# Optimization experiments

Measured on AMD Instinct MI355X. Metric: run time of the kernel, lower is better.

The kernel has to match this reference:

```python
import jax, jax.numpy as jnp
import numpy as np

D = 128  # time-encoder dimension == attention embed_dim


def harmonic_encode(ts, basis_freq):
    # ts: (N,) -> (N, D); phases are zero in the original module
    m = ts[:, None] * basis_freq[None, :]
    return jnp.sqrt(1.0 / D) * jnp.concatenate([jnp.cos(m), jnp.sin(m)], axis=1)


def mha_1head(q, k, mask, Wq, bq, Wk, bk, Wv, bv, Wo, bo):
    # Single-head nn.MultiheadAttention. q: (T, D) queries (torch batch dim),
    # k: (S, D) shared keys/values (original repeats these T times; same math),
    # mask: (T, S) True = masked out (key_padding_mask semantics).
    qp = q @ Wq.T + bq
    kp = k @ Wk.T + bk
    vp = k @ Wv.T + bv
    scores = jnp.einsum('td,sd->ts', qp, kp) / jnp.sqrt(jnp.asarray(D, q.dtype))
    scores = jnp.where(mask, -jnp.inf, scores)
    attn = jax.nn.softmax(scores, axis=-1)  # (T, S)
    return (attn @ vp) @ Wo.T + bo


def setup_inputs() -> dict:
    key = jax.random.key(0)
    ks = jax.random.split(key, 24)
    T, L, V = 4096, 8192, 1000
    s = 1.0 / np.sqrt(D)
    inp = {
        't': jax.random.uniform(ks[0], (T,), jnp.float32),
        'e_nodes_ts': jax.random.uniform(ks[1], (L,), jnp.float32),
        'e_nodes_exp': jax.random.randint(ks[2], (L,), 0, V),
        'e_node_target': jax.random.randint(ks[3], (1,), 0, V),
        'basis_freq': jnp.asarray(1.0 / 5.0 ** np.linspace(1, 9, D // 2), jnp.float32),
        'phi': jnp.ones((1,), jnp.float32),
        'W_lin': jax.random.normal(ks[4], (1, 2 * D), jnp.float32) * 0.05,
        'b_lin': jnp.zeros((1,), jnp.float32),
    }
    kidx = 5
    for suf in ('_s', '_n'):
        for nm in ('Wq', 'Wk', 'Wv', 'Wo'):
            inp[nm + suf] = jax.random.normal(ks[kidx], (D, D), jnp.float32) * s
            kidx += 1
        for nm in ('bq', 'bk', 'bv', 'bo'):
            inp[nm + suf] = jnp.zeros((D,), jnp.float32)
    return inp


def reference(t, e_nodes_ts, e_nodes_exp, e_node_target, basis_freq, phi, W_lin, b_lin,
              Wq_s, Wk_s, Wv_s, Wo_s, bq_s, bk_s, bv_s, bo_s,
              Wq_n, Wk_n, Wv_n, Wo_n, bq_n, bk_n, bv_n, bo_n):
    # prepend sentinels exactly as the torch forward does
    ts_all = jnp.concatenate([jnp.zeros((2,), e_nodes_ts.dtype), e_nodes_ts])      # (S,)
    exp_all = jnp.concatenate([jnp.full((1,), -1, e_nodes_exp.dtype), e_node_target, e_nodes_exp])  # (S,)

    phi_t = harmonic_encode(t, basis_freq)        # (T, D)
    phi_ts = harmonic_encode(ts_all, basis_freq)  # (S, D)

    pad = ts_all[None, :] > t[:, None]            # (T, S) future events masked
    self_mask = pad | (exp_all != e_node_target[0])[None, :]
    neig_mask = pad | (exp_all == e_node_target[0])[None, :]

    out_s = mha_1head(phi_t, phi_ts, self_mask, Wq_s, bq_s, Wk_s, bk_s, Wv_s, bv_s, Wo_s, bo_s)
    out_n = mha_1head(phi_t, phi_ts, neig_mask, Wq_n, bq_n, Wk_n, bk_n, Wv_n, bv_n, Wo_n, bo_n)
    atten_output = jnp.concatenate([out_s, out_n], axis=1)  # (T, 2D)

    lam = atten_output @ W_lin.T + b_lin          # (T, 1)
    x = lam * phi
    x = jnp.where(x > 20.0, 20.0, x)              # clamp as in soft_plus()
    lambdav = (1.0 / phi) * jnp.log1p(jnp.exp(x))
    return lambdav, atten_output
```

## Files before the change

kernel.cpp:

```cpp
#include <hip/hip_runtime.h>

#define T_Q 4096
#define S_TOT 8194
#define S_ALLOC 8256
#define SELF_CAP 128
#define NSEG 11
#define NSLOT 12
#define NTILE_N 129
#define SCALE 0.08838834764831843f
#define NEG_BIG -1.0e30f
#define TS_INF 3.0e38f

typedef __attribute__((ext_vector_type(8))) short short8;
typedef __attribute__((ext_vector_type(4))) float f32x4;
typedef __attribute__((ext_vector_type(4))) unsigned short ush4;
typedef unsigned short ush;
typedef unsigned int uint32;
typedef unsigned long long u64;

static __device__ __forceinline__ ush f2bf(float f) {
    unsigned int u = __float_as_uint(f);
    u += 0x7FFFu + ((u >> 16) & 1u);
    return (ush)(u >> 16);
}

__global__ __launch_bounds__(256) void prep_kernel(
    const float* __restrict__ t, const float* __restrict__ ets,
    const int* __restrict__ exps, const int* __restrict__ tgtp,
    const float* __restrict__ bf,
    const float* __restrict__ Wo_s, const float* __restrict__ Wv_s, const float* __restrict__ bv_s,
    const float* __restrict__ Wo_n, const float* __restrict__ Wv_n, const float* __restrict__ bv_n,
    const float* __restrict__ Wq_s, const float* __restrict__ Wq_n,
    const float* __restrict__ Wk_s, const float* __restrict__ Wk_n,
    ush* __restrict__ phi_t, ush* __restrict__ phi_ts,
    float* __restrict__ ts_pad, float* __restrict__ ts1, int* __restrict__ perm1,
    u64* __restrict__ maskbits, ush* __restrict__ Wb, float* __restrict__ bvo)
{
    __shared__ float red[256];
    __shared__ int swcnt[4];
    __shared__ int stot;
    int bid = blockIdx.x, tid = threadIdx.x;

    if (bid < 3088) {
        int R = bid * 4 + (tid >> 6);
        int j = tid & 63;
        float x; ush* dst;
        if (R < T_Q) { x = t[R]; dst = phi_t + (size_t)R * 128; }
        else {
            int s = R - T_Q;
            x = (s < 2) ? 0.0f : ((s < S_TOT) ? ets[s - 2] : 0.0f);
            dst = phi_ts + (size_t)s * 128;
        }
        float m = x * bf[j];
        dst[j]      = f2bf(cosf(m) * SCALE);
        dst[64 + j] = f2bf(sinf(m) * SCALE);
    } else if (bid == 3088) {
        int tgt = tgtp[0];
        for (int i = tid; i < S_ALLOC; i += 256)
            ts_pad[i] = (i < 2) ? 0.f : ((i < S_TOT) ? ets[i - 2] : TS_INF);
        int w4 = tid >> 6, lane = tid & 63;
        int cbeg = w4 * 33, cend = (w4 == 3) ? NTILE_N : (cbeg + 33);
        u64 ltm = ((u64)1 << lane) - 1ull;
        int cnt = 0;
        for (int ch = cbeg; ch < cend; ++ch) {
            int s = ch * 64 + lane;
            bool m = (s < S_TOT) && ((s == 1) || (s >= 2 && exps[s - 2] == tgt));
            u64 b = __ballot(m);
            if (lane == 0) maskbits[ch] = b;
            cnt += __popcll(b);
        }
        if (lane == 0) swcnt[w4] = cnt;
        __syncthreads();
        if (tid == 0) {
            int a = 0;
            #pragma unroll
            for (int i = 0; i < 4; ++i) { int tc = swcnt[i]; swcnt[i] = a; a += tc; }
            stot = a;
        }
        __syncthreads();
        int off2 = swcnt[w4];
        for (int ch = cbeg; ch < cend; ++ch) {
            int s = ch * 64 + lane;
            bool m = (s < S_TOT) && ((s == 1) || (s >= 2 && exps[s - 2] == tgt));
            u64 b = __ballot(m);
            if (m) {
                int p = off2 + __popcll(b & ltm);
                if (p < SELF_CAP) { perm1[p] = s; ts1[p] = (s >= 2) ? ets[s - 2] : 0.f; }
            }
            off2 += __popcll(b);
        }
        __syncthreads();
        int st = stot > SELF_CAP ? SELF_CAP : stot;
        for (int i = st + tid; i < SELF_CAP; i += 256) { perm1[i] = 0; ts1[i] = TS_INF; }
    } else if (bid < 3217) {
        int row = bid - 3089;
        int h = tid >> 7, col = tid & 127;
        const float* Wo = h ? Wo_n : Wo_s;
        const float* Wv = h ? Wv_n : Wv_s;
        const float* bv = h ? bv_n : bv_s;
        float acc = 0.f;
        for (int jj = 0; jj < 128; ++jj) acc += Wo[row * 128 + jj] * Wv[jj * 128 + col];
        Wb[(size_t)(4 + h) * 16384 + row * 128 + col] = f2bf(acc);
        red[tid] = Wo[row * 128 + col] * bv[col];
        __syncthreads();
        for (int off = 64; off > 0; off >>= 1) {
            if ((tid & 127) < off) red[tid] += red[tid + off];
            __syncthreads();
        }
        if ((tid & 127) == 0) bvo[h * 128 + row] = red[tid];
    } else {
        int idx = (bid - 3217) * 256 + tid;
        int which = idx >> 14, e = idx & 16383;
        const float* src;
        switch (which) {
            case 0: src = Wq_s; break; case 1: src = Wq_n; break;
            case 2: src = Wk_s; break; default: src = Wk_n; break;
        }
        Wb[idx] = f2bf(src[e]);
    }
}

__global__ __launch_bounds__(256) void proj_kernel(
    const ush* __restrict__ phi_ts, const ush* __restrict__ Wb,
    const float* __restrict__ bk_s, const float* __restrict__ bk_n,
    const float* __restrict__ bvo, const int* __restrict__ perm1,
    ush* __restrict__ kpc, ush* __restrict__ vpoT)
{
    int y = blockIdx.y;
    const float* b; int M; const int* perm = nullptr; int ldv = 0;
    ush* out = nullptr; ush* outT = nullptr;
    switch (y) {
        case 0: b = bk_s;      M = SELF_CAP; perm = perm1; out = kpc; break;
        case 1: b = bk_n;      M = S_ALLOC;  out = kpc + (size_t)SELF_CAP * 128; break;
        case 2: b = bvo;       M = SELF_CAP; perm = perm1; outT = vpoT; ldv = SELF_CAP; break;
        default:b = bvo + 128; M = S_ALLOC;  outT = vpoT + (size_t)SELF_CAP * 128; ldv = S_ALLOC; break;
    }
    int mbase = blockIdx.x * 64 + (int)(threadIdx.x >> 6) * 16;
    if (mbase >= M) return;
    int lane = threadIdx.x & 63, u = lane >> 4, c = lane & 15;
    const ush* arow = perm ? (phi_ts + (size_t)perm[mbase + c] * 128)
                           : (phi_ts + (size_t)(mbase + c) * 128);
    short8 af[4];
    #pragma unroll
    for (int ks = 0; ks < 4; ++ks) af[ks] = *(const short8*)(arow + ks * 32 + u * 8);
    const ush* W = Wb + (size_t)(y + 2) * 16384;
    #pragma unroll
    for (int nt = 0; nt < 8; ++nt) {
        int ncol = nt * 16 + c;
        float bval = b[ncol];
        f32x4 acc = {bval, bval, bval, bval};
        #pragma unroll
        for (int ks = 0; ks < 4; ++ks) {
            short8 bf8 = *(const short8*)(W + ncol * 128 + ks * 32 + u * 8);
            acc = __builtin_amdgcn_mfma_f32_16x16x32_bf16(af[ks], bf8, acc, 0, 0, 0);
        }
        if (outT) {
            ush4 pk;
            #pragma unroll
            for (int r = 0; r < 4; ++r) pk[r] = f2bf(acc[r]);
            *(ush4*)(outT + (size_t)ncol * ldv + mbase + u * 4) = pk;
        } else {
            #pragma unroll
            for (int r = 0; r < 4; ++r)
                out[(size_t)(mbase + u * 4 + r) * 128 + ncol] = f2bf(acc[r]);
        }
    }
}

__global__ __launch_bounds__(256, 3) void attn_kernel(
    const ush* __restrict__ phi_t, const ush* __restrict__ kpc, const ush* __restrict__ vpoT,
    const ush* __restrict__ Wb,
    const float* __restrict__ bq_s, const float* __restrict__ bq_n,
    const float* __restrict__ ts_pad, const float* __restrict__ ts1,
    const u64* __restrict__ maskbits, const float* __restrict__ tq,
    float* __restrict__ Opart, float* __restrict__ mpart, float* __restrict__ lpart)
{
    int bid = blockIdx.x;
    int head, seg, qt, slot, t0, t1;
    if (bid < NSEG * 64) {
        head = 1; seg = bid % NSEG; qt = bid / NSEG; slot = seg;
        t0 = seg * NTILE_N / NSEG; t1 = (seg + 1) * NTILE_N / NSEG;
    } else {
        head = 0; seg = 0; qt = bid - NSEG * 64; slot = NSEG;
        t0 = 0; t1 = SELF_CAP / 64;
    }
    const ush* kph = kpc  + (head ? (size_t)SELF_CAP * 128 : 0);
    const ush* vph = vpoT + (head ? (size_t)SELF_CAP * 128 : 0);
    int ldv = head ? S_ALLOC : SELF_CAP;
    const float* tsh = head ? ts_pad : ts1;

    __shared__ __align__(16) ush K2[2][64 * 128];
    __shared__ __align__(16) ush V1[128 * 64];
    __shared__ float tsb[2][64];

    int tid = threadIdx.x, w = tid >> 6, lane = tid & 63;
    int u = lane >> 4, c = lane & 15;
    int qrow0 = qt * 64 + w * 16;

    short8 qf[4];
    {
        const ush* Wq = Wb + (size_t)(head ? 1 : 0) * 16384;
        const float* bq = head ? bq_n : bq_s;
        const ush* ar = phi_t + (size_t)(qrow0 + c) * 128;
        short8 af[4];
        #pragma unroll
        for (int ks = 0; ks < 4; ++ks) af[ks] = *(const short8*)(ar + ks * 32 + u * 8);
        ush* qstage = &K2[1][0];
        #pragma unroll
        for (int nt = 0; nt < 8; ++nt) {
            int ncol = nt * 16 + c;
            float bb = bq[ncol];
            f32x4 acc = {bb, bb, bb, bb};
            #pragma unroll
            for (int ks = 0; ks < 4; ++ks) {
                short8 wf = *(const short8*)(Wq + ncol * 128 + ks * 32 + u * 8);
                acc = __builtin_amdgcn_mfma_f32_16x16x32_bf16(af[ks], wf, acc, 0, 0, 0);
            }
            #pragma unroll
            for (int r = 0; r < 4; ++r) {
                int lr = w * 16 + u * 4 + r;
                qstage[lr * 128 + (((ncol >> 3) ^ (lr & 7)) << 3) + (ncol & 7)] = f2bf(acc[r]);
            }
        }
        __syncthreads();
        int lr2 = w * 16 + c;
        #pragma unroll
        for (int ks = 0; ks < 4; ++ks)
            qf[ks] = *(const short8*)&qstage[lr2 * 128 + (((ks * 4 + u) ^ (lr2 & 7)) << 3)];
        __syncthreads();
    }
    float t_c = tq[qrow0 + c];

    f32x4 Ov[8];
    #pragma unroll
    for (int dt = 0; dt < 8; ++dt) Ov[dt] = (f32x4){0.f, 0.f, 0.f, 0.f};
    float mrow = NEG_BIG, lrow = 0.f;

    short8 kreg[4], vreg[4]; float tsreg = 0.f;
    int kr = tid >> 2, kq = tid & 3;
    int vd = tid >> 1, vh = tid & 1;
    int sbase = (lane & 48) + ((lane & 48) >> 2);

    auto LOADT = [&](int t) {
        int kb = t * 64;
        const ush* src = kph + (size_t)(kb + kr) * 128 + kq * 32;
        #pragma unroll
        for (int i = 0; i < 4; ++i) kreg[i] = *(const short8*)(src + i * 8);
        const ush* vsrc = vph + (size_t)vd * ldv + kb + vh * 32;
        #pragma unroll
        for (int i = 0; i < 4; ++i) vreg[i] = *(const short8*)(vsrc + i * 8);
        if (tid < 64) tsreg = tsh[kb + tid];
    };
    auto WRITE_K = [&](int b) {
        #pragma unroll
        for (int i = 0; i < 4; ++i)
            *(short8*)&K2[b][kr * 128 + (((kq * 4 + i) ^ (kr & 7)) << 3)] = kreg[i];
        if (tid < 64) tsb[b][tid] = tsreg;
    };
    auto WRITE_V = [&]() {
        #pragma unroll
        for (int i = 0; i < 4; ++i)
            *(short8*)&V1[vd * 64 + (((vh * 4 + i) ^ (vd & 7)) << 3)] = vreg[i];
    };

    LOADT(t0); WRITE_K(0); WRITE_V();
    __syncthreads();

    for (int t = t0; t < t1; ++t) {
        int cur = (t - t0) & 1;
        bool pre = (t + 1 < t1);
        u64 mk = head ? maskbits[t] : 0ull;
        if (pre) LOADT(t + 1);

        float sc[4][4];
        #pragma unroll
        for (int ct = 0; ct < 4; ++ct) {
            f32x4 acc = {0.f, 0.f, 0.f, 0.f};
            int row = ct * 16 + c;
            #pragma unroll
            for (int ks = 0; ks < 4; ++ks) {
                short8 kf = *(const short8*)&K2[cur][row * 128 + (((ks * 4 + u) ^ (row & 7)) << 3)];
                acc = __builtin_amdgcn_mfma_f32_16x16x32_bf16(kf, qf[ks], acc, 0, 0, 0);
            }
            f32x4 ts4 = *(const f32x4*)&tsb[cur][ct * 16 + u * 4];
            uint32 mh = (uint32)(mk >> (ct * 16 + u * 4));
            #pragma unroll
            for (int r = 0; r < 4; ++r) {
                bool bad = ((mh >> r) & 1u) || (ts4[r] > t_c);
                sc[ct][r] = bad ? NEG_BIG : acc[r] * SCALE;
            }
        }
        if (pre) WRITE_K(cur ^ 1);

        float mt = sc[0][0];
        #pragma unroll
        for (int ct = 0; ct < 4; ++ct)
            #pragma unroll
            for (int r = 0; r < 4; ++r) mt = fmaxf(mt, sc[ct][r]);
        mt = fmaxf(mt, __shfl_xor(mt, 16));
        mt = fmaxf(mt, __shfl_xor(mt, 32));
        if (__any(mt > mrow)) {
            float mnew = fmaxf(mrow, mt);
            float sf = __expf(mrow - mnew);
            mrow = mnew;
            lrow *= sf;
            float sfr[4];
            #pragma unroll
            for (int r = 0; r < 4; ++r) sfr[r] = __shfl(sf, sbase + r);
            #pragma unroll
            for (int dt = 0; dt < 8; ++dt) {
                Ov[dt][0] *= sfr[0]; Ov[dt][1] *= sfr[1];
                Ov[dt][2] *= sfr[2]; Ov[dt][3] *= sfr[3];
            }
        }
        float p[4][4];
        float s16 = 0.f;
        #pragma unroll
        for (int ct = 0; ct < 4; ++ct)
            #pragma unroll
            for (int r = 0; r < 4; ++r) { p[ct][r] = __expf(sc[ct][r] - mrow); s16 += p[ct][r]; }
        s16 += __shfl_xor(s16, 16);
        s16 += __shfl_xor(s16, 32);
        lrow += s16;

        uint32 q0[4], q1[4];
        #pragma unroll
        for (int ct = 0; ct < 4; ++ct) {
            asm("v_cvt_pk_bf16_f32 %0, %1, %2" : "=v"(q0[ct]) : "v"(p[ct][0]), "v"(p[ct][1]));
            asm("v_cvt_pk_bf16_f32 %0, %1, %2" : "=v"(q1[ct]) : "v"(p[ct][2]), "v"(p[ct][3]));
        }
        short8 pf[2];
        #pragma unroll
        for (int ksl = 0; ksl < 2; ++ksl) {
            uint32 a0 = q0[2 * ksl], b0 = q0[2 * ksl + 1];
            uint32 a1 = q1[2 * ksl], b1 = q1[2 * ksl + 1];
            asm("v_permlane32_swap_b32 %0, %1" : "+v"(a0), "+v"(b0));
            asm("v_permlane16_swap_b32 %0, %1" : "+v"(a0), "+v"(b0));
            asm("v_permlane32_swap_b32 %0, %1" : "+v"(a1), "+v"(b1));
            asm("v_permlane16_swap_b32 %0, %1" : "+v"(a1), "+v"(b1));
            union { uint32 w4[4]; short8 s8; } pk_;
            pk_.w4[0] = a0; pk_.w4[1] = a1; pk_.w4[2] = b0; pk_.w4[3] = b1;
            pf[ksl] = pk_.s8;
        }

        #pragma unroll
        for (int ksl = 0; ksl < 2; ++ksl)
            #pragma unroll
            for (int dt = 0; dt < 8; ++dt) {
                int d = dt * 16 + c;
                short8 vf = *(const short8*)&V1[d * 64 + (((ksl * 4 + u) ^ (d & 7)) << 3)];
                Ov[dt] = __builtin_amdgcn_mfma_f32_16x16x32_bf16(pf[ksl], vf, Ov[dt], 0, 0, 0);
            }

        __syncthreads();
        if (pre) WRITE_V();
        __syncthreads();
    }

    size_t rbase = (size_t)slot * T_Q + qrow0;
    #pragma unroll
    for (int dt = 0; dt < 8; ++dt)
        #pragma unroll
        for (int r = 0; r < 4; ++r)
            Opart[(rbase + u * 4 + r) * 128 + dt * 16 + c] = Ov[dt][r];
    if (lane < 16) {
        mpart[rbase + lane] = mrow;
        lpart[rbase + lane] = lrow;
    }
}

__global__ __launch_bounds__(256) void combine_kernel(
    const float* __restrict__ Opart, const float* __restrict__ mpart, const float* __restrict__ lpart,
    const float* __restrict__ bo_s, const float* __restrict__ bo_n,
    const float* __restrict__ Wl, const float* __restrict__ bl,
    const float* __restrict__ phi, float* __restrict__ outp)
{
    int row = blockIdx.x, tid = threadIdx.x;
    float outv;
    if (tid < 128) {
        size_t rb = (size_t)NSEG * T_Q + row;
        outv = Opart[rb * 128 + tid] / lpart[rb] + bo_s[tid];
    } else {
        int d = tid - 128;
        float M = NEG_BIG;
        #pragma unroll
        for (int z = 0; z < NSEG; ++z) M = fmaxf(M, mpart[(size_t)z * T_Q + row]);
        float L = 0.f, O = 0.f;
        #pragma unroll
        for (int z = 0; z < NSEG; ++z) {
            size_t rb = (size_t)z * T_Q + row;
            float wz = __expf(mpart[rb] - M);
            L += wz * lpart[rb];
            O += wz * Opart[rb * 128 + d];
        }
        outv = O / L + bo_n[d];
    }
    outp[T_Q + (size_t)row * 256 + tid] = outv;

    float dot = outv * Wl[tid];
    #pragma unroll
    for (int off = 1; off < 64; off <<= 1) dot += __shfl_xor(dot, off);
    __shared__ float wsum[4];
    if ((tid & 63) == 0) wsum[tid >> 6] = dot;
    __syncthreads();
    if (tid == 0) {
        float s = wsum[0] + wsum[1] + wsum[2] + wsum[3];
        float ph = phi[0];
        float x = (s + bl[0]) * ph;
        x = fminf(x, 20.0f);
        outp[row] = log1pf(__expf(x)) / ph;
    }
}

extern "C" void kernel_launch(void* const* d_in, const int* in_sizes, int n_in,
                              void* d_out, int out_size, void* d_ws, size_t ws_size,
                              hipStream_t stream) {
    (void)in_sizes; (void)n_in; (void)out_size; (void)ws_size;
    const float* t    = (const float*)d_in[0];
    const float* ets  = (const float*)d_in[1];
    const int*   exps = (const int*)d_in[2];
    const int*   tgt  = (const int*)d_in[3];
    const float* bfq  = (const float*)d_in[4];
    const float* phi  = (const float*)d_in[5];
    const float* Wlin = (const float*)d_in[6];
    const float* blin = (const float*)d_in[7];
    const float* Wq_s = (const float*)d_in[8];
    const float* Wk_s = (const float*)d_in[9];
    const float* Wv_s = (const float*)d_in[10];
    const float* Wo_s = (const float*)d_in[11];
    const float* bq_s = (const float*)d_in[12];
    const float* bk_s = (const float*)d_in[13];
    const float* bv_s = (const float*)d_in[14];
    const float* bo_s = (const float*)d_in[15];
    const float* Wq_n = (const float*)d_in[16];
    const float* Wk_n = (const float*)d_in[17];
    const float* Wv_n = (const float*)d_in[18];
    const float* Wo_n = (const float*)d_in[19];
    const float* bq_n = (const float*)d_in[20];
    const float* bk_n = (const float*)d_in[21];
    const float* bv_n = (const float*)d_in[22];
    const float* bo_n = (const float*)d_in[23];

    char* ws = (char*)d_ws;
    size_t off = 0;
    auto alloc = [&](size_t bytes) { void* p = ws + off; off += (bytes + 255) & ~(size_t)255; return p; };
    ush* phi_t  = (ush*)alloc((size_t)T_Q * 128 * 2);
    ush* phi_ts = (ush*)alloc((size_t)S_ALLOC * 128 * 2);
    ush* kpc    = (ush*)alloc((size_t)(SELF_CAP + S_ALLOC) * 128 * 2);
    ush* vpoT   = (ush*)alloc((size_t)128 * (SELF_CAP + S_ALLOC) * 2);
    int*   perm1 = (int*)  alloc((size_t)SELF_CAP * 4);
    float* ts1   = (float*)alloc((size_t)SELF_CAP * 4);
    float* ts_pad= (float*)alloc((size_t)S_ALLOC * 4);
    u64*  maskb  = (u64*)  alloc((size_t)NTILE_N * 8);
    float* bvo   = (float*)alloc((size_t)2 * 128 * 4);
    ush*   Wb    = (ush*)  alloc((size_t)6 * 16384 * 2);
    float* Opart = (float*)alloc((size_t)NSLOT * T_Q * 128 * 4);
    float* mpart = (float*)alloc((size_t)NSLOT * T_Q * 4);
    float* lpart = (float*)alloc((size_t)NSLOT * T_Q * 4);

    float* outp = (float*)d_out;

    prep_kernel<<<dim3(3473), dim3(256), 0, stream>>>(
        t, ets, exps, tgt, bfq, Wo_s, Wv_s, bv_s, Wo_n, Wv_n, bv_n,
        Wq_s, Wq_n, Wk_s, Wk_n, phi_t, phi_ts, ts_pad, ts1, perm1, maskb, Wb, bvo);
    proj_kernel<<<dim3(129, 4), dim3(256), 0, stream>>>(
        phi_ts, Wb, bk_s, bk_n, bvo, perm1, kpc, vpoT);
    attn_kernel<<<dim3(NSEG * 64 + 64), dim3(256), 0, stream>>>(
        phi_t, kpc, vpoT, Wb, bq_s, bq_n, ts_pad, ts1, maskb, t, Opart, mpart, lpart);
    combine_kernel<<<dim3(T_Q), dim3(256), 0, stream>>>(
        Opart, mpart, lpart, bo_s, bo_n, Wlin, blin, phi, outp);
}
```

Before: 107.4 us.

## Move Q projection to proj kernel; single-wave attention blocks reading K/V from global

```diff
diff --git a/kernel.cpp b/kernel.cpp
--- a/kernel.cpp
+++ b/kernel.cpp
@@ -4,9 +4,10 @@
 #define S_TOT 8194
 #define S_ALLOC 8256
 #define SELF_CAP 128
-#define NSEG 11
-#define NSLOT 12
-#define NTILE_N 129
+#define NSEG 15
+#define NSLOT 16
+#define NCH64 129
+#define NT32 258
 #define SCALE 0.08838834764831843f
 #define NEG_BIG -1.0e30f
 #define TS_INF 3.0e38f
@@ -34,7 +35,7 @@
     const float* __restrict__ Wk_s, const float* __restrict__ Wk_n,
     ush* __restrict__ phi_t, ush* __restrict__ phi_ts,
     float* __restrict__ ts_pad, float* __restrict__ ts1, int* __restrict__ perm1,
-    u64* __restrict__ maskbits, ush* __restrict__ Wb, float* __restrict__ bvo)
+    uint32* __restrict__ mask32, ush* __restrict__ Wb, float* __restrict__ bvo)
 {
     __shared__ float red[256];
     __shared__ int swcnt[4];
@@ -59,14 +60,14 @@
         for (int i = tid; i < S_ALLOC; i += 256)
             ts_pad[i] = (i < 2) ? 0.f : ((i < S_TOT) ? ets[i - 2] : TS_INF);
         int w4 = tid >> 6, lane = tid & 63;
-        int cbeg = w4 * 33, cend = (w4 == 3) ? NTILE_N : (cbeg + 33);
+        int cbeg = w4 * 33, cend = (w4 == 3) ? NCH64 : (cbeg + 33);
         u64 ltm = ((u64)1 << lane) - 1ull;
         int cnt = 0;
         for (int ch = cbeg; ch < cend; ++ch) {
             int s = ch * 64 + lane;
             bool m = (s < S_TOT) && ((s == 1) || (s >= 2 && exps[s - 2] == tgt));
             u64 b = __ballot(m);
-            if (lane == 0) maskbits[ch] = b;
+            if (lane == 0) { mask32[ch * 2] = (uint32)b; mask32[ch * 2 + 1] = (uint32)(b >> 32); }
             cnt += __popcll(b);
         }
         if (lane == 0) swcnt[w4] = cnt;
@@ -121,29 +122,33 @@
 }
 
 __global__ __launch_bounds__(256) void proj_kernel(
-    const ush* __restrict__ phi_ts, const ush* __restrict__ Wb,
+    const ush* __restrict__ phi_t, const ush* __restrict__ phi_ts, const ush* __restrict__ Wb,
+    const float* __restrict__ bq_s, const float* __restrict__ bq_n,
     const float* __restrict__ bk_s, const float* __restrict__ bk_n,
     const float* __restrict__ bvo, const int* __restrict__ perm1,
-    ush* __restrict__ kpc, ush* __restrict__ vpoT)
+    ush* __restrict__ qp, ush* __restrict__ kpc, ush* __restrict__ vpoT)
 {
     int y = blockIdx.y;
     const float* b; int M; const int* perm = nullptr; int ldv = 0;
+    const ush* in = phi_ts;
     ush* out = nullptr; ush* outT = nullptr;
     switch (y) {
-        case 0: b = bk_s;      M = SELF_CAP; perm = perm1; out = kpc; break;
-        case 1: b = bk_n;      M = S_ALLOC;  out = kpc + (size_t)SELF_CAP * 128; break;
-        case 2: b = bvo;       M = SELF_CAP; perm = perm1; outT = vpoT; ldv = SELF_CAP; break;
+        case 0: b = bq_s;      M = T_Q; in = phi_t; out = qp; break;
+        case 1: b = bq_n;      M = T_Q; in = phi_t; out = qp + (size_t)T_Q * 128; break;
+        case 2: b = bk_s;      M = SELF_CAP; perm = perm1; out = kpc; break;
+        case 3: b = bk_n;      M = S_ALLOC;  out = kpc + (size_t)SELF_CAP * 128; break;
+        case 4: b = bvo;       M = SELF_CAP; perm = perm1; outT = vpoT; ldv = SELF_CAP; break;
         default:b = bvo + 128; M = S_ALLOC;  outT = vpoT + (size_t)SELF_CAP * 128; ldv = S_ALLOC; break;
     }
     int mbase = blockIdx.x * 64 + (int)(threadIdx.x >> 6) * 16;
     if (mbase >= M) return;
     int lane = threadIdx.x & 63, u = lane >> 4, c = lane & 15;
-    const ush* arow = perm ? (phi_ts + (size_t)perm[mbase + c] * 128)
-                           : (phi_ts + (size_t)(mbase + c) * 128);
+    const ush* arow = perm ? (in + (size_t)perm[mbase + c] * 128)
+                           : (in + (size_t)(mbase + c) * 128);
     short8 af[4];
     #pragma unroll
     for (int ks = 0; ks < 4; ++ks) af[ks] = *(const short8*)(arow + ks * 32 + u * 8);
-    const ush* W = Wb + (size_t)(y + 2) * 16384;
+    const ush* W = Wb + (size_t)y * 16384;
     #pragma unroll
     for (int nt = 0; nt < 8; ++nt) {
         int ncol = nt * 16 + c;
@@ -167,205 +172,142 @@
     }
 }
 
-__global__ __launch_bounds__(256, 3) void attn_kernel(
-    const ush* __restrict__ phi_t, const ush* __restrict__ kpc, const ush* __restrict__ vpoT,
-    const ush* __restrict__ Wb,
-    const float* __restrict__ bq_s, const float* __restrict__ bq_n,
+__global__ __launch_bounds__(64, 2) void attn_kernel(
+    const ush* __restrict__ qp, const ush* __restrict__ kpc, const ush* __restrict__ vpoT,
     const float* __restrict__ ts_pad, const float* __restrict__ ts1,
-    const u64* __restrict__ maskbits, const float* __restrict__ tq,
+    const uint32* __restrict__ mask32, const float* __restrict__ tq,
     float* __restrict__ Opart, float* __restrict__ mpart, float* __restrict__ lpart)
 {
     int bid = blockIdx.x;
-    int head, seg, qt, slot, t0, t1;
-    if (bid < NSEG * 64) {
-        head = 1; seg = bid % NSEG; qt = bid / NSEG; slot = seg;
-        t0 = seg * NTILE_N / NSEG; t1 = (seg + 1) * NTILE_N / NSEG;
+    int head, qw, slot, t0, t1;
+    if (bid < 128 * NSEG) {
+        head = 1; int seg = bid % NSEG; qw = bid / NSEG; slot = seg;
+        t0 = seg * NT32 / NSEG; t1 = (seg + 1) * NT32 / NSEG;
     } else {
-        head = 0; seg = 0; qt = bid - NSEG * 64; slot = NSEG;
-        t0 = 0; t1 = SELF_CAP / 64;
+        head = 0; qw = bid - 128 * NSEG; slot = NSEG; t0 = 0; t1 = SELF_CAP / 32;
     }
     const ush* kph = kpc  + (head ? (size_t)SELF_CAP * 128 : 0);
     const ush* vph = vpoT + (head ? (size_t)SELF_CAP * 128 : 0);
-    int ldv = head ? S_ALLOC : SELF_CAP;
+    const int ldk = head ? S_ALLOC : SELF_CAP;
     const float* tsh = head ? ts_pad : ts1;
-
-    __shared__ __align__(16) ush K2[2][64 * 128];
-    __shared__ __align__(16) ush V1[128 * 64];
-    __shared__ float tsb[2][64];
-
-    int tid = threadIdx.x, w = tid >> 6, lane = tid & 63;
+    const ush* qph = qp + (head ? (size_t)T_Q * 128 : 0);
+
+    int lane = threadIdx.x;
     int u = lane >> 4, c = lane & 15;
-    int qrow0 = qt * 64 + w * 16;
-
-    short8 qf[4];
-    {
-        const ush* Wq = Wb + (size_t)(head ? 1 : 0) * 16384;
-        const float* bq = head ? bq_n : bq_s;
-        const ush* ar = phi_t + (size_t)(qrow0 + c) * 128;
-        short8 af[4];
-        #pragma unroll
-        for (int ks = 0; ks < 4; ++ks) af[ks] = *(const short8*)(ar + ks * 32 + u * 8);
-        ush* qstage = &K2[1][0];
-        #pragma unroll
-        for (int nt = 0; nt < 8; ++nt) {
-            int ncol = nt * 16 + c;
-            float bb = bq[ncol];
-            f32x4 acc = {bb, bb, bb, bb};
+    int qrow0 = qw * 32;
+
+    short8 qf[2][4];
+    #pragma unroll
+    for (int qg = 0; qg < 2; ++qg) {
+        const ush* qr = qph + (size_t)(qrow0 + qg * 16 + c) * 128;
+        #pragma unroll
+        for (int ks = 0; ks < 4; ++ks) qf[qg][ks] = *(const short8*)(qr + ks * 32 + u * 8);
+    }
+    float t_c[2] = { tq[qrow0 + c], tq[qrow0 + 16 + c] };
+
+    f32x4 Ov[2][8];
+    #pragma unroll
+    for (int qg = 0; qg < 2; ++qg)
+        #pragma unroll
+        for (int dt = 0; dt < 8; ++dt) Ov[qg][dt] = (f32x4){0.f, 0.f, 0.f, 0.f};
+    float mrow[2] = {NEG_BIG, NEG_BIG}, lrow[2] = {0.f, 0.f};
+    int sbase = (lane & 48) + ((lane & 48) >> 2);
+
+    for (int t = t0; t < t1; ++t) {
+        int kb = t * 32;
+        short8 kf0[4], kf1[4];
+        const ush* kr0 = kph + (size_t)(kb + c) * 128 + u * 8;
+        #pragma unroll
+        for (int ks = 0; ks < 4; ++ks) {
+            kf0[ks] = *(const short8*)(kr0 + ks * 32);
+            kf1[ks] = *(const short8*)(kr0 + 16 * 128 + ks * 32);
+        }
+        short8 vf[8];
+        const ush* vr = vph + (size_t)c * ldk + kb + u * 8;
+        #pragma unroll
+        for (int dt = 0; dt < 8; ++dt) vf[dt] = *(const short8*)(vr + (size_t)dt * 16 * ldk);
+        f32x4 tsa = *(const f32x4*)(tsh + kb + u * 4);
+        f32x4 tsc = *(const f32x4*)(tsh + kb + 16 + u * 4);
+        uint32 mk = head ? mask32[t] : 0u;
+
+        float sc[2][2][4];
+        #pragma unroll
+        for (int qg = 0; qg < 2; ++qg) {
+            f32x4 acc0 = {0.f, 0.f, 0.f, 0.f}, acc1 = {0.f, 0.f, 0.f, 0.f};
             #pragma unroll
             for (int ks = 0; ks < 4; ++ks) {
-                short8 wf = *(const short8*)(Wq + ncol * 128 + ks * 32 + u * 8);
-                acc = __builtin_amdgcn_mfma_f32_16x16x32_bf16(af[ks], wf, acc, 0, 0, 0);
+                acc0 = __builtin_amdgcn_mfma_f32_16x16x32_bf16(kf0[ks], qf[qg][ks], acc0, 0, 0, 0);
+                acc1 = __builtin_amdgcn_mfma_f32_16x16x32_bf16(kf1[ks], qf[qg][ks], acc1, 0, 0, 0);
             }
             #pragma unroll
             for (int r = 0; r < 4; ++r) {
-                int lr = w * 16 + u * 4 + r;
-                qstage[lr * 128 + (((ncol >> 3) ^ (lr & 7)) << 3) + (ncol & 7)] = f2bf(acc[r]);
+                bool bad0 = ((mk >> (u * 4 + r)) & 1u) || (tsa[r] > t_c[qg]);
+                bool bad1 = ((mk >> (16 + u * 4 + r)) & 1u) || (tsc[r] > t_c[qg]);
+                sc[qg][0][r] = bad0 ? NEG_BIG : acc0[r] * SCALE;
+                sc[qg][1][r] = bad1 ? NEG_BIG : acc1[r] * SCALE;
             }
         }
-        __syncthreads();
-        int lr2 = w * 16 + c;
-        #pragma unroll
-        for (int ks = 0; ks < 4; ++ks)
-            qf[ks] = *(const short8*)&qstage[lr2 * 128 + (((ks * 4 + u) ^ (lr2 & 7)) << 3)];
-        __syncthreads();
-    }
-    float t_c = tq[qrow0 + c];
-
-    f32x4 Ov[8];
-    #pragma unroll
-    for (int dt = 0; dt < 8; ++dt) Ov[dt] = (f32x4){0.f, 0.f, 0.f, 0.f};
-    float mrow = NEG_BIG, lrow = 0.f;
-
-    short8 kreg[4], vreg[4]; float tsreg = 0.f;
-    int kr = tid >> 2, kq = tid & 3;
-    int vd = tid >> 1, vh = tid & 1;
-    int sbase = (lane & 48) + ((lane & 48) >> 2);
-
-    auto LOADT = [&](int t) {
-        int kb = t * 64;
-        const ush* src = kph + (size_t)(kb + kr) * 128 + kq * 32;
-        #pragma unroll
-        for (int i = 0; i < 4; ++i) kreg[i] = *(const short8*)(src + i * 8);
-        const ush* vsrc = vph + (size_t)vd * ldv + kb + vh * 32;
-        #pragma unroll
-        for (int i = 0; i < 4; ++i) vreg[i] = *(const short8*)(vsrc + i * 8);
-        if (tid < 64) tsreg = tsh[kb + tid];
-    };
-    auto WRITE_K = [&](int b) {
-        #pragma unroll
-        for (int i = 0; i < 4; ++i)
-            *(short8*)&K2[b][kr * 128 + (((kq * 4 + i) ^ (kr & 7)) << 3)] = kreg[i];
-        if (tid < 64) tsb[b][tid] = tsreg;
-    };
-    auto WRITE_V = [&]() {
-        #pragma unroll
-        for (int i = 0; i < 4; ++i)
-            *(short8*)&V1[vd * 64 + (((vh * 4 + i) ^ (vd & 7)) << 3)] = vreg[i];
-    };
-
-    LOADT(t0); WRITE_K(0); WRITE_V();
-    __syncthreads();
-
-    for (int t = t0; t < t1; ++t) {
-        int cur = (t - t0) & 1;
-        bool pre = (t + 1 < t1);
-        u64 mk = head ? maskbits[t] : 0ull;
-        if (pre) LOADT(t + 1);
-
-        float sc[4][4];
-        #pragma unroll
-        for (int ct = 0; ct < 4; ++ct) {
-            f32x4 acc = {0.f, 0.f, 0.f, 0.f};
-            int row = ct * 16 + c;
-            #pragma unroll
-            for (int ks = 0; ks < 4; ++ks) {
-                short8 kf = *(const short8*)&K2[cur][row * 128 + (((ks * 4 + u) ^ (row & 7)) << 3)];
-                acc = __builtin_amdgcn_mfma_f32_16x16x32_bf16(kf, qf[ks], acc, 0, 0, 0);
+        #pragma unroll
+        for (int qg = 0; qg < 2; ++qg) {
+            float mt = fmaxf(fmaxf(fmaxf(sc[qg][0][0], sc[qg][0][1]), fmaxf(sc[qg][0][2], sc[qg][0][3])),
+                             fmaxf(fmaxf(sc[qg][1][0], sc[qg][1][1]), fmaxf(sc[qg][1][2], sc[qg][1][3])));
+            mt = fmaxf(mt, __shfl_xor(mt, 16));
+            mt = fmaxf(mt, __shfl_xor(mt, 32));
+            if (__any(mt > mrow[qg])) {
+                float mnew = fmaxf(mrow[qg], mt);
+                float sf = __expf(mrow[qg] - mnew);
+                mrow[qg] = mnew;
+                lrow[qg] *= sf;
+                float sfr[4];
+                #pragma unroll
+                for (int r = 0; r < 4; ++r) sfr[r] = __shfl(sf, sbase + r);
+                #pragma unroll
+                for (int dt = 0; dt < 8; ++dt) {
+                    Ov[qg][dt][0] *= sfr[0]; Ov[qg][dt][1] *= sfr[1];
+                    Ov[qg][dt][2] *= sfr[2]; Ov[qg][dt][3] *= sfr[3];
+                }
             }
-            f32x4 ts4 = *(const f32x4*)&tsb[cur][ct * 16 + u * 4];
-            uint32 mh = (uint32)(mk >> (ct * 16 + u * 4));
+            float p0[4], p1[4], s16 = 0.f;
             #pragma unroll
             for (int r = 0; r < 4; ++r) {
-                bool bad = ((mh >> r) & 1u) || (ts4[r] > t_c);
-                sc[ct][r] = bad ? NEG_BIG : acc[r] * SCALE;
+                p0[r] = __expf(sc[qg][0][r] - mrow[qg]);
+                p1[r] = __expf(sc[qg][1][r] - mrow[qg]);
+                s16 += p0[r] + p1[r];
             }
-        }
-        if (pre) WRITE_K(cur ^ 1);
-
-        float mt = sc[0][0];
-        #pragma unroll
-        for (int ct = 0; ct < 4; ++ct)
-            #pragma unroll
-            for (int r = 0; r < 4; ++r) mt = fmaxf(mt, sc[ct][r]);
-        mt = fmaxf(mt, __shfl_xor(mt, 16));
-        mt = fmaxf(mt, __shfl_xor(mt, 32));
-        if (__any(mt > mrow)) {
-            float mnew = fmaxf(mrow, mt);
-            float sf = __expf(mrow - mnew);
-            mrow = mnew;
-            lrow *= sf;
-            float sfr[4];
-            #pragma unroll
-            for (int r = 0; r < 4; ++r) sfr[r] = __shfl(sf, sbase + r);
-            #pragma unroll
-            for (int dt = 0; dt < 8; ++dt) {
-                Ov[dt][0] *= sfr[0]; Ov[dt][1] *= sfr[1];
-                Ov[dt][2] *= sfr[2]; Ov[dt][3] *= sfr[3];
-            }
-        }
-        float p[4][4];
-        float s16 = 0.f;
-        #pragma unroll
-        for (int ct = 0; ct < 4; ++ct)
-            #pragma unroll
-            for (int r = 0; r < 4; ++r) { p[ct][r] = __expf(sc[ct][r] - mrow); s16 += p[ct][r]; }
-        s16 += __shfl_xor(s16, 16);
-        s16 += __shfl_xor(s16, 32);
-        lrow += s16;
-
-        uint32 q0[4], q1[4];
-        #pragma unroll
-        for (int ct = 0; ct < 4; ++ct) {
-            asm("v_cvt_pk_bf16_f32 %0, %1, %2" : "=v"(q0[ct]) : "v"(p[ct][0]), "v"(p[ct][1]));
-            asm("v_cvt_pk_bf16_f32 %0, %1, %2" : "=v"(q1[ct]) : "v"(p[ct][2]), "v"(p[ct][3]));
-        }
-        short8 pf[2];
-        #pragma unroll
-        for (int ksl = 0; ksl < 2; ++ksl) {
-            uint32 a0 = q0[2 * ksl], b0 = q0[2 * ksl + 1];
-            uint32 a1 = q1[2 * ksl], b1 = q1[2 * ksl + 1];
+            s16 += __shfl_xor(s16, 16);
+            s16 += __shfl_xor(s16, 32);
+            lrow[qg] += s16;
+
+            uint32 a0, b0, a1, b1;
+            asm("v_cvt_pk_bf16_f32 %0, %1, %2" : "=v"(a0) : "v"(p0[0]), "v"(p0[1]));
+            asm("v_cvt_pk_bf16_f32 %0, %1, %2" : "=v"(b0) : "v"(p1[0]), "v"(p1[1]));
+            asm("v_cvt_pk_bf16_f32 %0, %1, %2" : "=v"(a1) : "v"(p0[2]), "v"(p0[3]));
+            asm("v_cvt_pk_bf16_f32 %0, %1, %2" : "=v"(b1) : "v"(p1[2]), "v"(p1[3]));
             asm("v_permlane32_swap_b32 %0, %1" : "+v"(a0), "+v"(b0));
             asm("v_permlane16_swap_b32 %0, %1" : "+v"(a0), "+v"(b0));
             asm("v_permlane32_swap_b32 %0, %1" : "+v"(a1), "+v"(b1));
             asm("v_permlane16_swap_b32 %0, %1" : "+v"(a1), "+v"(b1));
             union { uint32 w4[4]; short8 s8; } pk_;
             pk_.w4[0] = a0; pk_.w4[1] = a1; pk_.w4[2] = b0; pk_.w4[3] = b1;
-            pf[ksl] = pk_.s8;
-        }
-
-        #pragma unroll
-        for (int ksl = 0; ksl < 2; ++ksl)
-            #pragma unroll
-            for (int dt = 0; dt < 8; ++dt) {
-                int d = dt * 16 + c;
-                short8 vf = *(const short8*)&V1[d * 64 + (((ksl * 4 + u) ^ (d & 7)) << 3)];
-                Ov[dt] = __builtin_amdgcn_mfma_f32_16x16x32_bf16(pf[ksl], vf, Ov[dt], 0, 0, 0);
-            }
-
-        __syncthreads();
-        if (pre) WRITE_V();
-        __syncthreads();
+            short8 pf = pk_.s8;
+
+            #pragma unroll
+            for (int dt = 0; dt < 8; ++dt)
+                Ov[qg][dt] = __builtin_amdgcn_mfma_f32_16x16x32_bf16(pf, vf[dt], Ov[qg][dt], 0, 0, 0);
+        }
     }
 
     size_t rbase = (size_t)slot * T_Q + qrow0;
     #pragma unroll
-    for (int dt = 0; dt < 8; ++dt)
-        #pragma unroll
-        for (int r = 0; r < 4; ++r)
-            Opart[(rbase + u * 4 + r) * 128 + dt * 16 + c] = Ov[dt][r];
-    if (lane < 16) {
-        mpart[rbase + lane] = mrow;
-        lpart[rbase + lane] = lrow;
+    for (int qg = 0; qg < 2; ++qg)
+        #pragma unroll
+        for (int dt = 0; dt < 8; ++dt)
+            #pragma unroll
+            for (int r = 0; r < 4; ++r)
+                Opart[(rbase + qg * 16 + u * 4 + r) * 128 + dt * 16 + c] = Ov[qg][dt][r];
+    if (u == 0) {
+        mpart[rbase + c] = mrow[0];      lpart[rbase + c] = lrow[0];
+        mpart[rbase + 16 + c] = mrow[1]; lpart[rbase + 16 + c] = lrow[1];
     }
 }
 
@@ -446,27 +388,28 @@
     auto alloc = [&](size_t bytes) { void* p = ws + off; off += (bytes + 255) & ~(size_t)255; return p; };
     ush* phi_t  = (ush*)alloc((size_t)T_Q * 128 * 2);
     ush* phi_ts = (ush*)alloc((size_t)S_ALLOC * 128 * 2);
+    ush* qpb    = (ush*)alloc((size_t)2 * T_Q * 128 * 2);
     ush* kpc    = (ush*)alloc((size_t)(SELF_CAP + S_ALLOC) * 128 * 2);
     ush* vpoT   = (ush*)alloc((size_t)128 * (SELF_CAP + S_ALLOC) * 2);
-    int*   perm1 = (int*)  alloc((size_t)SELF_CAP * 4);
-    float* ts1   = (float*)alloc((size_t)SELF_CAP * 4);
-    float* ts_pad= (float*)alloc((size_t)S_ALLOC * 4);
-    u64*  maskb  = (u64*)  alloc((size_t)NTILE_N * 8);
-    float* bvo   = (float*)alloc((size_t)2 * 128 * 4);
-    ush*   Wb    = (ush*)  alloc((size_t)6 * 16384 * 2);
-    float* Opart = (float*)alloc((size_t)NSLOT * T_Q * 128 * 4);
-    float* mpart = (float*)alloc((size_t)NSLOT * T_Q * 4);
-    float* lpart = (float*)alloc((size_t)NSLOT * T_Q * 4);
+    int*    perm1 = (int*)   alloc((size_t)SELF_CAP * 4);
+    float*  ts1   = (float*) alloc((size_t)SELF_CAP * 4);
+    float*  ts_pad= (float*) alloc((size_t)S_ALLOC * 4);
+    uint32* maskb = (uint32*)alloc((size_t)NT32 * 4);
+    float*  bvo   = (float*) alloc((size_t)2 * 128 * 4);
+    ush*    Wb    = (ush*)   alloc((size_t)6 * 16384 * 2);
+    float*  Opart = (float*) alloc((size_t)NSLOT * T_Q * 128 * 4);
+    float*  mpart = (float*) alloc((size_t)NSLOT * T_Q * 4);
+    float*  lpart = (float*) alloc((size_t)NSLOT * T_Q * 4);
 
     float* outp = (float*)d_out;
 
     prep_kernel<<<dim3(3473), dim3(256), 0, stream>>>(
         t, ets, exps, tgt, bfq, Wo_s, Wv_s, bv_s, Wo_n, Wv_n, bv_n,
         Wq_s, Wq_n, Wk_s, Wk_n, phi_t, phi_ts, ts_pad, ts1, perm1, maskb, Wb, bvo);
-    proj_kernel<<<dim3(129, 4), dim3(256), 0, stream>>>(
-        phi_ts, Wb, bk_s, bk_n, bvo, perm1, kpc, vpoT);
-    attn_kernel<<<dim3(NSEG * 64 + 64), dim3(256), 0, stream>>>(
-        phi_t, kpc, vpoT, Wb, bq_s, bq_n, ts_pad, ts1, maskb, t, Opart, mpart, lpart);
+    proj_kernel<<<dim3(129, 6), dim3(256), 0, stream>>>(
+        phi_t, phi_ts, Wb, bq_s, bq_n, bk_s, bk_n, bvo, perm1, qpb, kpc, vpoT);
+    attn_kernel<<<dim3(128 * NSEG + 128), dim3(64), 0, stream>>>(
+        qpb, kpc, vpoT, ts_pad, ts1, maskb, t, Opart, mpart, lpart);
     combine_kernel<<<dim3(T_Q), dim3(256), 0, stream>>>(
         Opart, mpart, lpart, bo_s, bo_n, Wlin, blin, phi, outp);
 }
```

Measured after the change: 139.3 us. 1.3x slower.
